# Kernel optimization log

Hardware: AMD Instinct MI355X
Metric: run time of the kernel (lower is better)

Reference implementation:

```python
import jax, jax.numpy as jnp
import numpy as np

W, L, K, N = 32, 64, 512, 64


def setup_inputs() -> dict:
    key = jax.random.key(0)
    k0, k1, k2, k3 = jax.random.split(key, 4)
    # 0/1 spin states stored as float, matching torch.randint(0, 2, ..., dtype=float32)
    states = jax.random.randint(k0, (W, L, K, N), 0, 2).astype(jnp.float32)
    Q = jax.random.normal(k1, (W, N, N), dtype=jnp.float32)
    # inverse temperatures, ascending (standard parallel-tempering ladder)
    beta = jnp.sort(jax.random.uniform(k2, (L,), minval=0.1, maxval=2.0, dtype=jnp.float32))
    # uniform draws replacing torch.rand_like(delta) in exchange()
    u = jax.random.uniform(k3, (W, L - 1, K), dtype=jnp.float32)
    return {"states": states, "Q": Q, "beta": beta, "u": u}


def reference(states, Q, beta, u):
    """Temperer.exchange(): energies then masked replica swap.

    Returns (energies (W,L,K) before exchange, new states (W,L,K,N)).
    """
    # energy: einsum('wlki,wij,wlkj->wlk') done as one GEMM + elementwise reduce
    sQ = jnp.einsum('wlki,wij->wlkj', states, Q)          # (W,L,K,N)
    energies = jnp.einsum('wlkj,wlkj->wlk', sQ, states)   # (W,L,K)

    dbeta = (beta[1:] - beta[:-1])[None, :, None]          # (1,L-1,1)
    delta = (energies[:, 1:] - energies[:, :-1]) * dbeta   # (W,L-1,K)
    mask = (u < jnp.exp(delta)).astype(states.dtype)[..., None]  # (W,L-1,K,1)

    left = states[:, :-1]
    right = states[:, 1:]
    # replicate torch's sequential overlapping slice assignments exactly
    new = states.at[:, :-1].set(mask * right + (1.0 - mask) * left)
    new = new.at[:, 1:].set(mask * left + (1.0 - mask) * right)
    return energies, new
```

## Files before the change

### kernel.cpp

```cpp
#include <hip/hip_runtime.h>
#include <math.h>

#define PW 32
#define PL 64
#define PK 512
#define PN 64

typedef int   v4i __attribute__((ext_vector_type(4)));
typedef float v4f __attribute__((ext_vector_type(4)));


constexpr int ITERS_PER_WAVE = 4;

__global__ __launch_bounds__(256) void energies_kernel(
    const float* __restrict__ states, const float* __restrict__ Q,
    float* __restrict__ e_out, double* __restrict__ e64)
{
    __shared__ alignas(16) signed char Afrag[16 * 64 * 16];

    const int tid  = threadIdx.x;
    const int lane = tid & 63;
    const int wv   = tid >> 6;
    const int w    = blockIdx.x >> 6;
    const int blk  = blockIdx.x & 63;

    const float* Qw = Q + w * PN * PN;
    for (int e = tid; e < PN * PN; e += 256) {
        const int i = e >> 6, j = e & 63;
        long long R = llrint((double)Qw[e] * 268435456.0);
        const int frag_lane = ((i >> 4) << 4) | (j & 15);
        const int jt = j >> 4;
        const int b  = i & 15;
#pragma unroll
        for (int k = 0; k < 4; ++k) {
            const signed char d = (signed char)(R & 0xFF);
            R = (R - d) >> 8;
            Afrag[((k * 4 + jt) * 64 + frag_lane) * 16 + b] = d;
        }
    }
    __syncthreads();

    const v4i* Af = (const v4i*)Afrag;

    const long vw_base = (long)w * (PL * PK)
                       + (long)(blk * 4 + wv) * (32 * ITERS_PER_WAVE);

    for (int t = 0; t < ITERS_PER_WAVE; ++t) {
        const long vbase = vw_base + (long)t * 32;
        const float* sp = states + vbase * PN + lane;

        unsigned long long mkA = 0, mkB = 0;
#pragma unroll
        for (int v = 0; v < 16; ++v) {
            const float sA = sp[v * PN];
            const float sB = sp[(v + 16) * PN];
            const unsigned long long mA = __ballot(sA != 0.0f);
            const unsigned long long mB = __ballot(sB != 0.0f);
            const bool sel = (lane & 15) == v;
            mkA = sel ? mA : mkA;
            mkB = sel ? mB : mkB;
        }

        const int sh = (lane >> 4) * 16;
        const unsigned int bA = (unsigned int)(mkA >> sh) & 0xFFFFu;
        const unsigned int bB = (unsigned int)(mkB >> sh) & 0xFFFFu;
        v4i BA, BB;
#pragma unroll
        for (int q = 0; q < 4; ++q) {
            BA[q] = (int)((((bA >> (4 * q)) & 0xFu) * 0x00204081u) & 0x01010101u);
            BB[q] = (int)((((bB >> (4 * q)) & 0xFu) * 0x00204081u) & 0x01010101u);
        }

        int selA[4], selB[4];
#pragma unroll
        for (int jt = 0; jt < 4; ++jt) {
            selA[jt] = (int)((mkA >> (jt * 16 + ((lane >> 4) * 4))) & 0xF);
            selB[jt] = (int)((mkB >> (jt * 16 + ((lane >> 4) * 4))) & 0xF);
        }

        long long accA = 0, accB = 0;
#pragma unroll
        for (int k = 0; k < 4; ++k) {
            v4i A0 = Af[(k * 4 + 0) * 64 + lane];
            v4i A1 = Af[(k * 4 + 1) * 64 + lane];
            v4i A2 = Af[(k * 4 + 2) * 64 + lane];
            v4i A3 = Af[(k * 4 + 3) * 64 + lane];
            v4i CA0 = {0,0,0,0}, CA1 = {0,0,0,0}, CA2 = {0,0,0,0}, CA3 = {0,0,0,0};
            v4i CB0 = {0,0,0,0}, CB1 = {0,0,0,0}, CB2 = {0,0,0,0}, CB3 = {0,0,0,0};
            asm("s_nop 1\n\t"
                "v_mfma_i32_16x16x64_i8 %0, %8, %12, %0\n\t"
                "v_mfma_i32_16x16x64_i8 %4, %8, %13, %4\n\t"
                "v_mfma_i32_16x16x64_i8 %1, %9, %12, %1\n\t"
                "v_mfma_i32_16x16x64_i8 %5, %9, %13, %5\n\t"
                "v_mfma_i32_16x16x64_i8 %2, %10, %12, %2\n\t"
                "v_mfma_i32_16x16x64_i8 %6, %10, %13, %6\n\t"
                "v_mfma_i32_16x16x64_i8 %3, %11, %12, %3\n\t"
                "v_mfma_i32_16x16x64_i8 %7, %11, %13, %7\n\t"
                "s_nop 7\n\t"
                "s_nop 7"
                : "+v"(CA0), "+v"(CA1), "+v"(CA2), "+v"(CA3),
                  "+v"(CB0), "+v"(CB1), "+v"(CB2), "+v"(CB3)
                : "v"(A0), "v"(A1), "v"(A2), "v"(A3), "v"(BA), "v"(BB));
            int akA = 0, akB = 0;
#pragma unroll
            for (int r = 0; r < 4; ++r) {
                akA += ((selA[0] >> r) & 1) * CA0[r];
                akA += ((selA[1] >> r) & 1) * CA1[r];
                akA += ((selA[2] >> r) & 1) * CA2[r];
                akA += ((selA[3] >> r) & 1) * CA3[r];
                akB += ((selB[0] >> r) & 1) * CB0[r];
                akB += ((selB[1] >> r) & 1) * CB1[r];
                akB += ((selB[2] >> r) & 1) * CB2[r];
                akB += ((selB[3] >> r) & 1) * CB3[r];
            }
            accA += (long long)akA << (8 * k);
            accB += (long long)akB << (8 * k);
        }

        accA += __shfl_xor(accA, 16, 64);
        accA += __shfl_xor(accA, 32, 64);
        accB += __shfl_xor(accB, 16, 64);
        accB += __shfl_xor(accB, 32, 64);

        if (lane < 16) {
            const double eA = (double)accA * 0x1p-28;
            const double eB = (double)accB * 0x1p-28;
            e64[vbase + lane]        = eA;
            e_out[vbase + lane]      = (float)eA;
            e64[vbase + 16 + lane]   = eB;
            e_out[vbase + 16 + lane] = (float)eB;
        }
    }
}

__global__ __launch_bounds__(256) void mask_kernel(
    const double* __restrict__ e64, const float* __restrict__ beta,
    const float* __restrict__ u, unsigned char* __restrict__ mask)
{
    const int idx = blockIdx.x * blockDim.x + threadIdx.x;
    if (idx >= PW * (PL - 1) * PK) return;
    const int k = idx % PK;
    const int m = (idx / PK) % (PL - 1);
    const int w = idx / (PK * (PL - 1));
    const long e1 = ((long)w * PL + m) * PK + k;
    const double db = (double)beta[m + 1] - (double)beta[m];
    const double delta = (e64[e1 + PK] - e64[e1]) * db;
    mask[idx] = ((double)u[idx] < exp(delta)) ? 1 : 0;
}

__global__ __launch_bounds__(256) void swap_kernel(
    const float* __restrict__ states, const unsigned char* __restrict__ mask,
    float* __restrict__ out)
{
    const long rowBase = (long)blockIdx.x * 32;
    const int w  = (int)(rowBase >> 15);
    const int l  = (int)((rowBase >> 9) & 63);
    const int k0 = (int)(rowBase & 511);

    const int tid = threadIdx.x;
    const int r  = tid >> 3;
    const int j4 = tid & 7;
    const int k  = k0 + r;

    const int ml = (l == 0) ? 0 : (l - 1);
    const unsigned char mk = mask[((long)w * (PL - 1) + ml) * PK + k];
    int sl;
    if (l == 0) sl = mk ? 1 : 0;
    else        sl = mk ? (l - 1) : l;

    const v4f* srcp = (const v4f*)(states + (((long)w * PL + sl) * PK + k) * PN);
    v4f*       dstp = (v4f*)(out + (rowBase + r) * PN);
    __builtin_nontemporal_store(srcp[j4],     &dstp[j4]);
    __builtin_nontemporal_store(srcp[j4 + 8], &dstp[j4 + 8]);
}

extern "C" void kernel_launch(void* const* d_in, const int* in_sizes, int n_in,
                              void* d_out, int out_size, void* d_ws, size_t ws_size,
                              hipStream_t stream) {
    const float* states = (const float*)d_in[0];
    const float* Q      = (const float*)d_in[1];
    const float* beta   = (const float*)d_in[2];
    const float* u      = (const float*)d_in[3];

    float* e_out      = (float*)d_out;
    float* new_states = (float*)d_out + (long)PW * PL * PK;

    double* e64 = (double*)d_ws;
    unsigned char* mask = (unsigned char*)d_ws + sizeof(double) * (long)PW * PL * PK;

    energies_kernel<<<2048, 256, 0, stream>>>(states, Q, e_out, e64);

    const int nmask = PW * (PL - 1) * PK;
    mask_kernel<<<(nmask + 255) / 256, 256, 0, stream>>>(e64, beta, u, mask);

    swap_kernel<<<32768, 256, 0, stream>>>(states, mask, new_states);
}
```

Baseline: 523.8 us.

## Pre-pack spin states into bitmasks in a separate kernel before energy MFMA

Adds a pack kernel that reads states with coalesced float4 loads and ballots them into one 64-bit bitmask per replica, stored in workspace. The energy kernel now reads these bitmasks instead of doing 32 strided scalar loads and ballots per iteration, and the Q fragment layout and the selector bit extraction are remapped to match the new bit ordering. The swap kernel also drops nontemporal stores in favour of plain float4 copies. The cost is an extra launch plus a bitmask write and read through global memory.

```diff
diff --git a/kernel.cpp b/kernel.cpp
--- a/kernel.cpp
+++ b/kernel.cpp
@@ -10,10 +10,42 @@
 typedef float v4f __attribute__((ext_vector_type(4)));
 
 
+__global__ __launch_bounds__(256) void pack_kernel(
+    const float* __restrict__ states, unsigned long long* __restrict__ pmask)
+{
+    const int lane = threadIdx.x & 63;
+    const long wave = ((long)blockIdx.x * blockDim.x + threadIdx.x) >> 6;
+    const long vb = wave * 16;
+
+    unsigned long long pm = 0;
+#pragma unroll
+    for (int it = 0; it < 4; ++it) {
+        const v4f* gp = (const v4f*)(states + (vb + it * 4) * PN);
+        const v4f f = gp[lane];
+        const unsigned long long m0 = __ballot(f.x != 0.0f);
+        const unsigned long long m1 = __ballot(f.y != 0.0f);
+        const unsigned long long m2 = __ballot(f.z != 0.0f);
+        const unsigned long long m3 = __ballot(f.w != 0.0f);
+        unsigned long long mm[4];
+#pragma unroll
+        for (int vv = 0; vv < 4; ++vv) {
+            mm[vv] = ((m0 >> (vv * 16)) & 0xFFFFull)
+                   | (((m1 >> (vv * 16)) & 0xFFFFull) << 16)
+                   | (((m2 >> (vv * 16)) & 0xFFFFull) << 32)
+                   | (((m3 >> (vv * 16)) & 0xFFFFull) << 48);
+        }
+        const unsigned long long s01 = (lane & 1) ? mm[1] : mm[0];
+        const unsigned long long s23 = (lane & 1) ? mm[3] : mm[2];
+        const unsigned long long sel = (lane & 2) ? s23 : s01;
+        pm = ((lane >> 2) == it) ? sel : pm;
+    }
+    if (lane < 16) pmask[vb + lane] = pm;
+}
+
 constexpr int ITERS_PER_WAVE = 4;
 
 __global__ __launch_bounds__(256) void energies_kernel(
-    const float* __restrict__ states, const float* __restrict__ Q,
+    const unsigned long long* __restrict__ pmask, const float* __restrict__ Q,
     float* __restrict__ e_out, double* __restrict__ e64)
 {
     __shared__ alignas(16) signed char Afrag[16 * 64 * 16];
@@ -28,9 +60,9 @@
     for (int e = tid; e < PN * PN; e += 256) {
         const int i = e >> 6, j = e & 63;
         long long R = llrint((double)Qw[e] * 268435456.0);
-        const int frag_lane = ((i >> 4) << 4) | (j & 15);
+        const int h = i & 3, b = i >> 2;
+        const int frag_lane = (h << 4) | (j & 15);
         const int jt = j >> 4;
-        const int b  = i & 15;
 #pragma unroll
         for (int k = 0; k < 4; ++k) {
             const signed char d = (signed char)(R & 0xFF);
@@ -44,38 +76,31 @@
 
     const long vw_base = (long)w * (PL * PK)
                        + (long)(blk * 4 + wv) * (32 * ITERS_PER_WAVE);
+    const int h = lane >> 4;
 
     for (int t = 0; t < ITERS_PER_WAVE; ++t) {
         const long vbase = vw_base + (long)t * 32;
-        const float* sp = states + vbase * PN + lane;
-
-        unsigned long long mkA = 0, mkB = 0;
-#pragma unroll
-        for (int v = 0; v < 16; ++v) {
-            const float sA = sp[v * PN];
-            const float sB = sp[(v + 16) * PN];
-            const unsigned long long mA = __ballot(sA != 0.0f);
-            const unsigned long long mB = __ballot(sB != 0.0f);
-            const bool sel = (lane & 15) == v;
-            mkA = sel ? mA : mkA;
-            mkB = sel ? mB : mkB;
-        }
-
-        const int sh = (lane >> 4) * 16;
-        const unsigned int bA = (unsigned int)(mkA >> sh) & 0xFFFFu;
-        const unsigned int bB = (unsigned int)(mkB >> sh) & 0xFFFFu;
+
+        const unsigned long long pmA = pmask[vbase + (lane & 15)];
+        const unsigned long long pmB = pmask[vbase + 16 + (lane & 15)];
+
+        const unsigned int bA = (unsigned int)(pmA >> (h * 16)) & 0xFFFFu;
+        const unsigned int bB = (unsigned int)(pmB >> (h * 16)) & 0xFFFFu;
         v4i BA, BB;
 #pragma unroll
         for (int q = 0; q < 4; ++q) {
             BA[q] = (int)((((bA >> (4 * q)) & 0xFu) * 0x00204081u) & 0x01010101u);
+            BB[q] = (int)((((bB >> (4 * q)) & 0xFu) * 0x01010101u >> 0) & 0x01010101u);
+        }
+#pragma unroll
+        for (int q = 0; q < 4; ++q)
             BB[q] = (int)((((bB >> (4 * q)) & 0xFu) * 0x00204081u) & 0x01010101u);
-        }
-
-        int selA[4], selB[4];
-#pragma unroll
-        for (int jt = 0; jt < 4; ++jt) {
-            selA[jt] = (int)((mkA >> (jt * 16 + ((lane >> 4) * 4))) & 0xF);
-            selB[jt] = (int)((mkB >> (jt * 16 + ((lane >> 4) * 4))) & 0xF);
+
+        unsigned int xA[4], xB[4];
+#pragma unroll
+        for (int r = 0; r < 4; ++r) {
+            xA[r] = (unsigned int)(pmA >> (r * 16 + h)) & 0x1111u;
+            xB[r] = (unsigned int)(pmB >> (r * 16 + h)) & 0x1111u;
         }
 
         long long accA = 0, accB = 0;
@@ -104,14 +129,14 @@
             int akA = 0, akB = 0;
 #pragma unroll
             for (int r = 0; r < 4; ++r) {
-                akA += ((selA[0] >> r) & 1) * CA0[r];
-                akA += ((selA[1] >> r) & 1) * CA1[r];
-                akA += ((selA[2] >> r) & 1) * CA2[r];
-                akA += ((selA[3] >> r) & 1) * CA3[r];
-                akB += ((selB[0] >> r) & 1) * CB0[r];
-                akB += ((selB[1] >> r) & 1) * CB1[r];
-                akB += ((selB[2] >> r) & 1) * CB2[r];
-                akB += ((selB[3] >> r) & 1) * CB3[r];
+                akA += ((xA[r] >> 0)  & 1) * CA0[r];
+                akA += ((xA[r] >> 4)  & 1) * CA1[r];
+                akA += ((xA[r] >> 8)  & 1) * CA2[r];
+                akA += ((xA[r] >> 12) & 1) * CA3[r];
+                akB += ((xB[r] >> 0)  & 1) * CB0[r];
+                akB += ((xB[r] >> 4)  & 1) * CB1[r];
+                akB += ((xB[r] >> 8)  & 1) * CB2[r];
+                akB += ((xB[r] >> 12) & 1) * CB3[r];
             }
             accA += (long long)akA << (8 * k);
             accB += (long long)akB << (8 * k);
@@ -168,10 +193,10 @@
     if (l == 0) sl = mk ? 1 : 0;
     else        sl = mk ? (l - 1) : l;
 
-    const v4f* srcp = (const v4f*)(states + (((long)w * PL + sl) * PK + k) * PN);
-    v4f*       dstp = (v4f*)(out + (rowBase + r) * PN);
-    __builtin_nontemporal_store(srcp[j4],     &dstp[j4]);
-    __builtin_nontemporal_store(srcp[j4 + 8], &dstp[j4 + 8]);
+    const float4* srcp = (const float4*)(states + (((long)w * PL + sl) * PK + k) * PN);
+    float4*       dstp = (float4*)(out + (rowBase + r) * PN);
+    dstp[j4]     = srcp[j4];
+    dstp[j4 + 8] = srcp[j4 + 8];
 }
 
 extern "C" void kernel_launch(void* const* d_in, const int* in_sizes, int n_in,
@@ -185,10 +210,14 @@
     float* e_out      = (float*)d_out;
     float* new_states = (float*)d_out + (long)PW * PL * PK;
 
+    const long NV = (long)PW * PL * PK;
     double* e64 = (double*)d_ws;
-    unsigned char* mask = (unsigned char*)d_ws + sizeof(double) * (long)PW * PL * PK;
-
-    energies_kernel<<<2048, 256, 0, stream>>>(states, Q, e_out, e64);
+    unsigned long long* pmask = (unsigned long long*)((char*)d_ws + 8 * NV);
+    unsigned char* mask = (unsigned char*)d_ws + 16 * NV;
+
+    pack_kernel<<<16384, 256, 0, stream>>>(states, pmask);
+
+    energies_kernel<<<2048, 256, 0, stream>>>(pmask, Q, e_out, e64);
 
     const int nmask = PW * (PL - 1) * PK;
     mask_kernel<<<(nmask + 255) / 256, 256, 0, stream>>>(e64, beta, u, mask);
```

Result: no change. 526.2 us (+0.5%).
